# Optimization experiments

Hardware: AMD Instinct MI355X
Metric: run time of the kernel (lower is better)

Reference implementation:

```python
import jax, jax.numpy as jnp
import numpy as np

B, Q, N, C = 16, 200, 200, 64   # batch, queries, candidates, edge classes
T = 100                          # matched targets per batch (len of prev_permutation_indices entries)
G, S = 50, 4                     # target groups per batch, edges per group (col_ids sizes)


def setup_inputs() -> dict:
    key = jax.random.key(0)
    k0, k1, k2, k3, k4 = jax.random.split(key, 5)
    batch_edges = jax.random.normal(k0, (B, Q, N, C), dtype=jnp.float32)
    query_indices = jax.random.randint(k1, (B, T), 0, N)           # index into N dim
    target_indices = jax.random.randint(k2, (B, T), 0, 10000)      # ordering keys, argsorted
    col_ids = jax.random.randint(k3, (B, G, S), 0, T)              # index into matched-target dim
    edge_target_indices = jax.random.randint(k4, (B, G, S), 0, C)  # class labels per edge
    return {
        "batch_edges": batch_edges,
        "query_indices": query_indices,
        "target_indices": target_indices,
        "col_ids": col_ids,
        "edge_target_indices": edge_target_indices,
    }


def reference(batch_edges, query_indices, target_indices, col_ids, edge_target_indices):
    # softmax over edge classes
    probs = jax.nn.softmax(batch_edges, axis=-1)                       # [B,Q,N,C]
    # sorted_query_indices = query_indices[argsort(target_indices)] per batch
    order = jnp.argsort(target_indices, axis=-1)                       # [B,T]
    sq = jnp.take_along_axis(query_indices, order, axis=-1)            # [B,T]
    # valid_edges = edges[:, prev_query_indices, :]
    valid = jnp.take_along_axis(probs, sq[:, None, :, None], axis=2)   # [B,Q,T,C]
    # all_edges = valid_edges[:, col_indices, :]  (col_ids flattened over groups)
    col_flat = col_ids.reshape(B, G * S)                               # [B,G*S]
    all_e = jnp.take_along_axis(valid, col_flat[:, None, :, None], axis=2)  # [B,Q,G*S,C]
    # pick target class per edge, negate, sum within each group
    tgt_flat = edge_target_indices.reshape(B, G * S)                   # [B,G*S]
    picked = jnp.take_along_axis(all_e, tgt_flat[:, None, :, None], axis=3)[..., 0]  # [B,Q,G*S]
    cost = -picked.reshape(B, Q, G, S).sum(axis=-1)                    # [B,Q,G]
    # torch.cat over batches along last dim -> [Q, B*G], then expand to [B,Q,B*G]
    cat = cost.transpose(1, 0, 2).reshape(Q, B * G)
    return jnp.broadcast_to(cat[None, :, :], (B, Q, B * G))
```

## Files before the change

kernel.cpp:

```cpp
#include <hip/hip_runtime.h>

#define BB 16
#define QQ 200
#define NN 200
#define CC 64
#define TT 100
#define GG 50
#define SS 4
#define EE (GG*SS)
#define QPB 2

__global__ __launch_bounds__(256) void edge_cost_fused_kernel(
    const float* __restrict__ edges,
    const int* __restrict__ query_indices,
    const int* __restrict__ target_indices,
    const int* __restrict__ col_ids,
    const int* __restrict__ edge_tgt,
    float* __restrict__ out)
{
    const int blk = blockIdx.x;
    const int b  = blk / (QQ / QPB);
    const int q0 = (blk % (QQ / QPB)) * QPB;
    const int tid = threadIdx.x;

    __shared__ int   tk[TT];
    __shared__ int   qi[TT];
    __shared__ int   order_sh[TT];
    __shared__ int   ep_sh[EE];
    __shared__ float sm_sh[QPB][TT];
    __shared__ float cost_sh[QPB][GG];

    if (tid < TT) {
        tk[tid] = target_indices[b * TT + tid];
        qi[tid] = query_indices[b * TT + tid];
    }
    if (tid < EE) {
        const int t_e = col_ids[b * EE + tid];
        const int c_e = edge_tgt[b * EE + tid];
        ep_sh[tid] = t_e * 64 + c_e;
    }

    const float* base = edges + ((size_t)(b * QQ + q0)) * NN * CC;
    const int* qi_g = query_indices + b * TT;

    const int grp  = tid >> 4;
    const int lane = tid & 15;
    #pragma unroll
    for (int it = 0; it < 7; ++it) {
        const int t = grp + it * 16;
        if (t < TT) {
            const int n = qi_g[t];
            const float* r0 = base + (size_t)n * CC;
            const float4 v0 = reinterpret_cast<const float4*>(r0)[lane];
            const float4 v1 = reinterpret_cast<const float4*>(r0 + NN * CC)[lane];
            float e0 = __expf(v0.x) + __expf(v0.y) + __expf(v0.z) + __expf(v0.w);
            float e1 = __expf(v1.x) + __expf(v1.y) + __expf(v1.z) + __expf(v1.w);
            #pragma unroll
            for (int off = 1; off < 16; off <<= 1) {
                e0 += __shfl_xor(e0, off, 64);
                e1 += __shfl_xor(e1, off, 64);
            }
            if (lane == 0) { sm_sh[0][t] = e0; sm_sh[1][t] = e1; }
        }
    }
    __syncthreads();

    if (tid < TT) {
        const int key = tk[tid];
        int rank = 0;
        #pragma unroll 4
        for (int j = 0; j < TT; ++j) {
            const int kj = tk[j];
            rank += (kj < key) || (kj == key && j < tid);
        }
        order_sh[rank] = tid;
    }
    __syncthreads();

    if (tid < EE) {
        const int pack = ep_sh[tid];
        const int t_e = pack >> 6;
        const int c   = pack & 63;
        const int o   = order_sh[t_e];
        const size_t roff = (size_t)qi[o] * CC + c;
        const float x0 = base[roff];
        const float x1 = base[(size_t)NN * CC + roff];
        float p0 = __expf(x0) / sm_sh[0][o];
        float p1 = __expf(x1) / sm_sh[1][o];
        p0 += __shfl_xor(p0, 1, 64);  p1 += __shfl_xor(p1, 1, 64);
        p0 += __shfl_xor(p0, 2, 64);  p1 += __shfl_xor(p1, 2, 64);
        if ((tid & 3) == 0) {
            cost_sh[0][tid >> 2] = -p0;
            cost_sh[1][tid >> 2] = -p1;
        }
    }
    __syncthreads();

    for (int i = tid; i < QPB * BB * GG; i += 256) {
        const int qq = i / (BB * GG);
        const int r  = i % (BB * GG);
        const int b2 = r / GG;
        const int g  = r % GG;
        out[((size_t)b2 * QQ + q0 + qq) * (BB * GG) + b * GG + g] = cost_sh[qq][g];
    }
}

extern "C" void kernel_launch(void* const* d_in, const int* in_sizes, int n_in,
                              void* d_out, int out_size, void* d_ws, size_t ws_size,
                              hipStream_t stream) {
    const float* edges = (const float*)d_in[0];
    const int* query_indices  = (const int*)d_in[1];
    const int* target_indices = (const int*)d_in[2];
    const int* col_ids        = (const int*)d_in[3];
    const int* edge_tgt       = (const int*)d_in[4];
    float* out = (float*)d_out;

    edge_cost_fused_kernel<<<BB * (QQ / QPB), 256, 0, stream>>>(
        edges, query_indices, target_indices, col_ids, edge_tgt, out);
}
```

Baseline: 25.97 us.

## Split fused kernel into sort-pack, stats-gather, and coalesced replicate kernels

Moves the per-batch argsort and index packing into a small pre-kernel, so the sort is no longer recomputed in every one of the 1600 blocks. The main kernel now runs 800 blocks that each process two work items and write compact costs to workspace. A third kernel replicates the cost across the batch dimension with coalesced writes instead of scattered stores. This adds two extra launches and a workspace round trip.

Measured after the change: 34.89 us. +34.3%, slower.

```diff
diff --git a/kernel.cpp b/kernel.cpp
--- a/kernel.cpp
+++ b/kernel.cpp
@@ -8,63 +8,22 @@
 #define GG 50
 #define SS 4
 #define EE (GG*SS)
-#define QPB 2
 
-__global__ __launch_bounds__(256) void edge_cost_fused_kernel(
-    const float* __restrict__ edges,
+
+__global__ __launch_bounds__(128) void sort_pack_kernel(
     const int* __restrict__ query_indices,
     const int* __restrict__ target_indices,
     const int* __restrict__ col_ids,
     const int* __restrict__ edge_tgt,
-    float* __restrict__ out)
+    int* __restrict__ epack)
 {
-    const int blk = blockIdx.x;
-    const int b  = blk / (QQ / QPB);
-    const int q0 = (blk % (QQ / QPB)) * QPB;
+    const int b = blockIdx.x;
     const int tid = threadIdx.x;
+    __shared__ int tk[TT];
+    __shared__ int order_sh[TT];
 
-    __shared__ int   tk[TT];
-    __shared__ int   qi[TT];
-    __shared__ int   order_sh[TT];
-    __shared__ int   ep_sh[EE];
-    __shared__ float sm_sh[QPB][TT];
-    __shared__ float cost_sh[QPB][GG];
-
-    if (tid < TT) {
-        tk[tid] = target_indices[b * TT + tid];
-        qi[tid] = query_indices[b * TT + tid];
-    }
-    if (tid < EE) {
-        const int t_e = col_ids[b * EE + tid];
-        const int c_e = edge_tgt[b * EE + tid];
-        ep_sh[tid] = t_e * 64 + c_e;
-    }
-
-    const float* base = edges + ((size_t)(b * QQ + q0)) * NN * CC;
-    const int* qi_g = query_indices + b * TT;
-
-    const int grp  = tid >> 4;
-    const int lane = tid & 15;
-    #pragma unroll
-    for (int it = 0; it < 7; ++it) {
-        const int t = grp + it * 16;
-        if (t < TT) {
-            const int n = qi_g[t];
-            const float* r0 = base + (size_t)n * CC;
-            const float4 v0 = reinterpret_cast<const float4*>(r0)[lane];
-            const float4 v1 = reinterpret_cast<const float4*>(r0 + NN * CC)[lane];
-            float e0 = __expf(v0.x) + __expf(v0.y) + __expf(v0.z) + __expf(v0.w);
-            float e1 = __expf(v1.x) + __expf(v1.y) + __expf(v1.z) + __expf(v1.w);
-            #pragma unroll
-            for (int off = 1; off < 16; off <<= 1) {
-                e0 += __shfl_xor(e0, off, 64);
-                e1 += __shfl_xor(e1, off, 64);
-            }
-            if (lane == 0) { sm_sh[0][t] = e0; sm_sh[1][t] = e1; }
-        }
-    }
+    if (tid < TT) tk[tid] = target_indices[b * TT + tid];
     __syncthreads();
-
     if (tid < TT) {
         const int key = tk[tid];
         int rank = 0;
@@ -76,32 +35,92 @@
         order_sh[rank] = tid;
     }
     __syncthreads();
+    for (int e = tid; e < EE; e += 128) {
+        const int t_e = col_ids[b * EE + e];
+        const int c_e = edge_tgt[b * EE + e];
+        const int o   = order_sh[t_e];
+        const int n   = query_indices[b * TT + o];
+        epack[b * EE + e] = (o << 14) | (n << 6) | c_e;
+    }
+}
 
-    if (tid < EE) {
-        const int pack = ep_sh[tid];
-        const int t_e = pack >> 6;
-        const int c   = pack & 63;
-        const int o   = order_sh[t_e];
-        const size_t roff = (size_t)qi[o] * CC + c;
-        const float x0 = base[roff];
-        const float x1 = base[(size_t)NN * CC + roff];
-        float p0 = __expf(x0) / sm_sh[0][o];
-        float p1 = __expf(x1) / sm_sh[1][o];
-        p0 += __shfl_xor(p0, 1, 64);  p1 += __shfl_xor(p1, 1, 64);
-        p0 += __shfl_xor(p0, 2, 64);  p1 += __shfl_xor(p1, 2, 64);
-        if ((tid & 3) == 0) {
-            cost_sh[0][tid >> 2] = -p0;
-            cost_sh[1][tid >> 2] = -p1;
+__global__ __launch_bounds__(256) void stats_gather_kernel(
+    const float* __restrict__ edges,
+    const int* __restrict__ query_indices,
+    const int* __restrict__ epack,
+    float* __restrict__ cost)
+{
+    const int tid = threadIdx.x;
+    const int grp  = tid >> 4;
+    const int lane = tid & 15;
+
+    __shared__ int   ep_sh[EE];
+    __shared__ float sm_sh[2][TT];
+
+    #pragma unroll
+    for (int rep = 0; rep < 2; ++rep) {
+        const int item = blockIdx.x + rep * 800;
+        const int b  = item / (QQ / 2);
+        const int q0 = (item % (QQ / 2)) * 2;
+
+        if (tid < EE) ep_sh[tid] = epack[b * EE + tid];
+
+        const float* base = edges + ((size_t)(b * QQ + q0)) * NN * CC;
+        const int* qi_g = query_indices + b * TT;
+
+        #pragma unroll
+        for (int it = 0; it < 7; ++it) {
+            const int t = grp + it * 16;
+            if (t < TT) {
+                const int n = qi_g[t];
+                const float* r0 = base + (size_t)n * CC;
+                const float4 v0 = reinterpret_cast<const float4*>(r0)[lane];
+                const float4 v1 = reinterpret_cast<const float4*>(r0 + NN * CC)[lane];
+                float e0 = __expf(v0.x) + __expf(v0.y) + __expf(v0.z) + __expf(v0.w);
+                float e1 = __expf(v1.x) + __expf(v1.y) + __expf(v1.z) + __expf(v1.w);
+                #pragma unroll
+                for (int off = 1; off < 16; off <<= 1) {
+                    e0 += __shfl_xor(e0, off, 64);
+                    e1 += __shfl_xor(e1, off, 64);
+                }
+                if (lane == 0) { sm_sh[0][t] = e0; sm_sh[1][t] = e1; }
+            }
         }
+        __syncthreads();
+
+        if (tid < EE) {
+            const int pk = ep_sh[tid];
+            const int o = pk >> 14;
+            const int n = (pk >> 6) & 255;
+            const int c = pk & 63;
+            const size_t roff = (size_t)n * CC + c;
+            float p0 = __expf(base[roff]) / sm_sh[0][o];
+            float p1 = __expf(base[(size_t)NN * CC + roff]) / sm_sh[1][o];
+            p0 += __shfl_xor(p0, 1, 64);  p1 += __shfl_xor(p1, 1, 64);
+            p0 += __shfl_xor(p0, 2, 64);  p1 += __shfl_xor(p1, 2, 64);
+            if ((tid & 3) == 0) {
+                cost[((size_t)b * QQ + q0)     * GG + (tid >> 2)] = -p0;
+                cost[((size_t)b * QQ + q0 + 1) * GG + (tid >> 2)] = -p1;
+            }
+        }
+        __syncthreads();
     }
-    __syncthreads();
+}
 
-    for (int i = tid; i < QPB * BB * GG; i += 256) {
-        const int qq = i / (BB * GG);
-        const int r  = i % (BB * GG);
-        const int b2 = r / GG;
-        const int g  = r % GG;
-        out[((size_t)b2 * QQ + q0 + qq) * (BB * GG) + b * GG + g] = cost_sh[qq][g];
+__global__ __launch_bounds__(256) void replicate_kernel(
+    const float* __restrict__ cost,
+    float* __restrict__ out)
+{
+    int i = blockIdx.x * 256 + threadIdx.x;
+    if (i < QQ * BB * GG) {
+        const int q = i / (BB * GG);
+        const int j = i % (BB * GG);
+        const int bsrc = j / GG;
+        const int g    = j % GG;
+        const float v = cost[((size_t)bsrc * QQ + q) * GG + g];
+        #pragma unroll
+        for (int b2 = 0; b2 < BB; ++b2)
+            out[((size_t)b2 * QQ + q) * (BB * GG) + j] = v;
     }
 }
 
@@ -115,6 +134,11 @@
     const int* edge_tgt       = (const int*)d_in[4];
     float* out = (float*)d_out;
 
-    edge_cost_fused_kernel<<<BB * (QQ / QPB), 256, 0, stream>>>(
-        edges, query_indices, target_indices, col_ids, edge_tgt, out);
+    int*   epack = (int*)d_ws;
+    float* cost  = (float*)((char*)d_ws + BB * EE * sizeof(int));
+
+    sort_pack_kernel<<<BB, 128, 0, stream>>>(query_indices, target_indices,
+                                             col_ids, edge_tgt, epack);
+    stats_gather_kernel<<<800, 256, 0, stream>>>(edges, query_indices, epack, cost);
+    replicate_kernel<<<(QQ * BB * GG + 255) / 256, 256, 0, stream>>>(cost, out);
 }
```

## Split index sorting into prep kernel and gather rows in sorted query order

Applied to the files above, without the earlier changes.

Moves the per-batch argsort rank computation and edge index packing into a small prep kernel that writes a sorted row list and packed edge descriptors to workspace, so the 1600 main blocks no longer redo the sort. The row-sum pass now walks query rows in sorted order, which is meant to improve memory locality. The cost is an extra kernel launch and a dependency between the two kernels.

Result: slower. 29.78 us (+14.7%).

```diff
diff --git a/kernel.cpp b/kernel.cpp
--- a/kernel.cpp
+++ b/kernel.cpp
@@ -8,48 +8,76 @@
 #define GG 50
 #define SS 4
 #define EE (GG*SS)
-#define QPB 2
 
-__global__ __launch_bounds__(256) void edge_cost_fused_kernel(
-    const float* __restrict__ edges,
+
+__global__ __launch_bounds__(128) void prep_kernel(
     const int* __restrict__ query_indices,
     const int* __restrict__ target_indices,
     const int* __restrict__ col_ids,
     const int* __restrict__ edge_tgt,
-    float* __restrict__ out)
+    int* __restrict__ rowlist,
+    int* __restrict__ epack)
 {
-    const int blk = blockIdx.x;
-    const int b  = blk / (QQ / QPB);
-    const int q0 = (blk % (QQ / QPB)) * QPB;
+    const int b = blockIdx.x;
     const int tid = threadIdx.x;
-
-    __shared__ int   tk[TT];
-    __shared__ int   qi[TT];
-    __shared__ int   order_sh[TT];
-    __shared__ int   ep_sh[EE];
-    __shared__ float sm_sh[QPB][TT];
-    __shared__ float cost_sh[QPB][GG];
+    __shared__ int tk[TT], qi[TT];
+    __shared__ int order_sh[TT];
+    __shared__ int slotq[TT];
 
     if (tid < TT) {
         tk[tid] = target_indices[b * TT + tid];
         qi[tid] = query_indices[b * TT + tid];
     }
-    if (tid < EE) {
-        const int t_e = col_ids[b * EE + tid];
-        const int c_e = edge_tgt[b * EE + tid];
-        ep_sh[tid] = t_e * 64 + c_e;
+    __syncthreads();
+    if (tid < TT) {
+        const int kt = tk[tid], kq = qi[tid];
+        int rT = 0, rQ = 0;
+        #pragma unroll 4
+        for (int j = 0; j < TT; ++j) {
+            const int tj = tk[j], qj = qi[j];
+            rT += (tj < kt) || (tj == kt && j < tid);
+            rQ += (qj < kq) || (qj == kq && j < tid);
+        }
+        order_sh[rT] = tid;
+        slotq[tid] = rQ;
+        rowlist[b * TT + rQ] = kq;
     }
+    __syncthreads();
+    for (int e = tid; e < EE; e += 128) {
+        const int t_e = col_ids[b * EE + e];
+        const int c_e = edge_tgt[b * EE + e];
+        const int o   = order_sh[t_e];
+        epack[b * EE + e] = (slotq[o] << 14) | (qi[o] << 6) | c_e;
+    }
+}
+
+__global__ __launch_bounds__(256) void stats_gather_kernel(
+    const float* __restrict__ edges,
+    const int* __restrict__ rowlist,
+    const int* __restrict__ epack,
+    float* __restrict__ out)
+{
+    const int blk = blockIdx.x;
+    const int b  = blk / (QQ / 2);
+    const int q0 = (blk % (QQ / 2)) * 2;
+    const int tid = threadIdx.x;
+    const int grp  = tid >> 4;
+    const int lane = tid & 15;
+
+    __shared__ int   ep_sh[EE];
+    __shared__ float sm_sh[2][TT];
+    __shared__ float cost_sh[2][GG];
+
+    if (tid < EE) ep_sh[tid] = epack[b * EE + tid];
 
     const float* base = edges + ((size_t)(b * QQ + q0)) * NN * CC;
-    const int* qi_g = query_indices + b * TT;
+    const int* rl = rowlist + b * TT;
 
-    const int grp  = tid >> 4;
-    const int lane = tid & 15;
     #pragma unroll
     for (int it = 0; it < 7; ++it) {
         const int t = grp + it * 16;
         if (t < TT) {
-            const int n = qi_g[t];
+            const int n = rl[t];
             const float* r0 = base + (size_t)n * CC;
             const float4 v0 = reinterpret_cast<const float4*>(r0)[lane];
             const float4 v1 = reinterpret_cast<const float4*>(r0 + NN * CC)[lane];
@@ -65,28 +93,14 @@
     }
     __syncthreads();
 
-    if (tid < TT) {
-        const int key = tk[tid];
-        int rank = 0;
-        #pragma unroll 4
-        for (int j = 0; j < TT; ++j) {
-            const int kj = tk[j];
-            rank += (kj < key) || (kj == key && j < tid);
-        }
-        order_sh[rank] = tid;
-    }
-    __syncthreads();
-
     if (tid < EE) {
-        const int pack = ep_sh[tid];
-        const int t_e = pack >> 6;
-        const int c   = pack & 63;
-        const int o   = order_sh[t_e];
-        const size_t roff = (size_t)qi[o] * CC + c;
-        const float x0 = base[roff];
-        const float x1 = base[(size_t)NN * CC + roff];
-        float p0 = __expf(x0) / sm_sh[0][o];
-        float p1 = __expf(x1) / sm_sh[1][o];
+        const int pk = ep_sh[tid];
+        const int slot = pk >> 14;
+        const int n    = (pk >> 6) & 255;
+        const int c    = pk & 63;
+        const size_t roff = (size_t)n * CC + c;
+        float p0 = __expf(base[roff]) / sm_sh[0][slot];
+        float p1 = __expf(base[(size_t)NN * CC + roff]) / sm_sh[1][slot];
         p0 += __shfl_xor(p0, 1, 64);  p1 += __shfl_xor(p1, 1, 64);
         p0 += __shfl_xor(p0, 2, 64);  p1 += __shfl_xor(p1, 2, 64);
         if ((tid & 3) == 0) {
@@ -96,7 +110,7 @@
     }
     __syncthreads();
 
-    for (int i = tid; i < QPB * BB * GG; i += 256) {
+    for (int i = tid; i < 2 * BB * GG; i += 256) {
         const int qq = i / (BB * GG);
         const int r  = i % (BB * GG);
         const int b2 = r / GG;
@@ -115,6 +129,11 @@
     const int* edge_tgt       = (const int*)d_in[4];
     float* out = (float*)d_out;
 
-    edge_cost_fused_kernel<<<BB * (QQ / QPB), 256, 0, stream>>>(
-        edges, query_indices, target_indices, col_ids, edge_tgt, out);
+    int* rowlist = (int*)d_ws;
+    int* epack   = rowlist + BB * TT;
+
+    prep_kernel<<<BB, 128, 0, stream>>>(query_indices, target_indices,
+                                        col_ids, edge_tgt, rowlist, epack);
+    stats_gather_kernel<<<BB * (QQ / 2), 256, 0, stream>>>(edges, rowlist,
+                                                           epack, out);
 }
```

## Split fused kernel into cost computation and coalesced broadcast replication kernels

Applied to the files above, without the earlier changes.

The single fused kernel is split in two. The first computes the per-query group costs and writes them to a compact workspace buffer. The second kernel reads each cost once and writes it to all 16 batch copies of the output, so that stores along the last dimension are contiguous and coalesced instead of scattered 50-float segments from each block. This adds a second launch and a round trip through the workspace in global memory.

Measured after the change: 27.51 us. +5.9%, slower.

```diff
diff --git a/kernel.cpp b/kernel.cpp
--- a/kernel.cpp
+++ b/kernel.cpp
@@ -8,27 +8,27 @@
 #define GG 50
 #define SS 4
 #define EE (GG*SS)
-#define QPB 2
 
-__global__ __launch_bounds__(256) void edge_cost_fused_kernel(
+__global__ __launch_bounds__(256) void stats_gather_kernel(
     const float* __restrict__ edges,
     const int* __restrict__ query_indices,
     const int* __restrict__ target_indices,
     const int* __restrict__ col_ids,
     const int* __restrict__ edge_tgt,
-    float* __restrict__ out)
+    float* __restrict__ cost)
 {
     const int blk = blockIdx.x;
-    const int b  = blk / (QQ / QPB);
-    const int q0 = (blk % (QQ / QPB)) * QPB;
+    const int b  = blk / (QQ / 2);
+    const int q0 = (blk % (QQ / 2)) * 2;
     const int tid = threadIdx.x;
+    const int grp  = tid >> 4;
+    const int lane = tid & 15;
 
     __shared__ int   tk[TT];
     __shared__ int   qi[TT];
     __shared__ int   order_sh[TT];
     __shared__ int   ep_sh[EE];
-    __shared__ float sm_sh[QPB][TT];
-    __shared__ float cost_sh[QPB][GG];
+    __shared__ float sm_sh[2][TT];
 
     if (tid < TT) {
         tk[tid] = target_indices[b * TT + tid];
@@ -43,8 +43,6 @@
     const float* base = edges + ((size_t)(b * QQ + q0)) * NN * CC;
     const int* qi_g = query_indices + b * TT;
 
-    const int grp  = tid >> 4;
-    const int lane = tid & 15;
     #pragma unroll
     for (int it = 0; it < 7; ++it) {
         const int t = grp + it * 16;
@@ -83,25 +81,32 @@
         const int c   = pack & 63;
         const int o   = order_sh[t_e];
         const size_t roff = (size_t)qi[o] * CC + c;
-        const float x0 = base[roff];
-        const float x1 = base[(size_t)NN * CC + roff];
-        float p0 = __expf(x0) / sm_sh[0][o];
-        float p1 = __expf(x1) / sm_sh[1][o];
+        float p0 = __expf(base[roff]) / sm_sh[0][o];
+        float p1 = __expf(base[(size_t)NN * CC + roff]) / sm_sh[1][o];
         p0 += __shfl_xor(p0, 1, 64);  p1 += __shfl_xor(p1, 1, 64);
         p0 += __shfl_xor(p0, 2, 64);  p1 += __shfl_xor(p1, 2, 64);
         if ((tid & 3) == 0) {
-            cost_sh[0][tid >> 2] = -p0;
-            cost_sh[1][tid >> 2] = -p1;
+            const int g = tid >> 2;
+            cost[((size_t)b * QQ + q0)     * GG + g] = -p0;
+            cost[((size_t)b * QQ + q0 + 1) * GG + g] = -p1;
         }
     }
-    __syncthreads();
+}
 
-    for (int i = tid; i < QPB * BB * GG; i += 256) {
-        const int qq = i / (BB * GG);
-        const int r  = i % (BB * GG);
-        const int b2 = r / GG;
-        const int g  = r % GG;
-        out[((size_t)b2 * QQ + q0 + qq) * (BB * GG) + b * GG + g] = cost_sh[qq][g];
+__global__ __launch_bounds__(256) void replicate_kernel(
+    const float* __restrict__ cost,
+    float* __restrict__ out)
+{
+    int i = blockIdx.x * 256 + threadIdx.x;
+    if (i < QQ * BB * GG) {
+        const int q = i / (BB * GG);
+        const int j = i % (BB * GG);
+        const int bsrc = j / GG;
+        const int g    = j % GG;
+        const float v = cost[((size_t)bsrc * QQ + q) * GG + g];
+        #pragma unroll
+        for (int b2 = 0; b2 < BB; ++b2)
+            out[((size_t)b2 * QQ + q) * (BB * GG) + j] = v;
     }
 }
 
@@ -115,6 +120,9 @@
     const int* edge_tgt       = (const int*)d_in[4];
     float* out = (float*)d_out;
 
-    edge_cost_fused_kernel<<<BB * (QQ / QPB), 256, 0, stream>>>(
-        edges, query_indices, target_indices, col_ids, edge_tgt, out);
+    float* cost = (float*)d_ws;
+
+    stats_gather_kernel<<<BB * (QQ / 2), 256, 0, stream>>>(
+        edges, query_indices, target_indices, col_ids, edge_tgt, cost);
+    replicate_kernel<<<(QQ * BB * GG + 255) / 256, 256, 0, stream>>>(cost, out);
 }
```
